# Kernel optimization log

Measured on AMD Instinct MI355X. Metric: run time of the kernel, lower is better.

Reference implementation:

```python
import jax, jax.numpy as jnp
import numpy as np

KH, KW = 3, 3  # window_size[1], window_size[2]
SH, SW = 1, 1  # strides
FILTERS = 64


def _extract_patches(x, kh, kw, sh, sw):
    # TF tf.image.extract_patches ordering: depth = (row, col, channel), channel fastest.
    B, H, W, C = x.shape
    Ho = (H - kh) // sh + 1
    Wo = (W - kw) // sw + 1
    # stack kh*kw shifted views -> (B, Ho, Wo, kh*kw, C)
    views = [x[:, i:i + (Ho - 1) * sh + 1:sh, j:j + (Wo - 1) * sw + 1:sw, :]
             for i in range(kh) for j in range(kw)]
    patches = jnp.stack(views, axis=3)
    return patches.reshape(B, Ho, Wo, kh * kw * C)


def setup_inputs() -> dict:
    key = jax.random.key(0)
    k1, k2 = jax.random.split(key)
    B, H, W, C = 8, 32, 32, 32
    K = KH * KW * C  # 288
    x = jax.random.normal(k1, (B, H, W, C), dtype=jnp.float32)
    w = jax.random.normal(k2, (1, 1, 1, K, FILTERS), dtype=jnp.float32) * 0.05
    bias = jnp.zeros((FILTERS,), dtype=jnp.float32)
    return {"x": x, "w": w, "bias": bias}


def reference(x, w, bias):
    # patches: (B, Ho, Wo, K)
    patches = _extract_patches(x, KH, KW, SH, SW)
    # broadcast add: (B, Ho, Wo, K, F)
    s = patches[..., None] + w
    # tropical max-plus minus min-plus over the patch axis, plus bias
    return jnp.max(s, axis=3) - jnp.min(s, axis=3) + bias
```

## Files before the change

### kernel.cpp

```cpp
#include <hip/hip_runtime.h>
#include <math.h>


#define PIX 2
#define TPB 256

__global__ __launch_bounds__(TPB) void trop_kernel(
    const float* __restrict__ x,
    const float* __restrict__ w,
    const float* __restrict__ bias,
    float* __restrict__ out)
{
    __shared__ float wlds[2][32 * 64];

    const int tid  = threadIdx.x;
    const int lane = tid & 63;
    const int wv   = tid >> 6;

    const int pix0 = blockIdx.x * (4 * PIX) + wv * PIX;

    const float* xp[PIX];
#pragma unroll
    for (int p = 0; p < PIX; ++p) {
        const int pid = pix0 + p;
        const int wo = pid % 30;
        const int t  = pid / 30;
        const int ho = t % 30;
        const int b  = t / 30;
        xp[p] = x + (((b * 32 + ho) * 32) + wo) * 32;
    }

    float amax[PIX], amin[PIX];
#pragma unroll
    for (int p = 0; p < PIX; ++p) { amax[p] = -INFINITY; amin[p] = INFINITY; }

    {
        const float4* src = (const float4*)w;
        ((float4*)wlds[0])[tid]       = src[tid];
        ((float4*)wlds[0])[tid + 256] = src[tid + 256];
    }
    __syncthreads();

#pragma unroll
    for (int tap = 0; tap < 9; ++tap) {
        const int cur = tap & 1;
        const int nxt = cur ^ 1;

        const int ntap = (tap < 8) ? tap + 1 : 8;
        const float4* src = (const float4*)(w + ntap * 2048);
        const float4 r0 = src[tid];
        const float4 r1 = src[tid + 256];

        const int dy = tap / 3;
        const int dx = tap % 3;
        const int xoff = (dy * 32 + dx) * 32;

#pragma unroll
        for (int c = 0; c < 32; c += 4) {
            const float w0 = wlds[cur][(c + 0) * 64 + lane];
            const float w1 = wlds[cur][(c + 1) * 64 + lane];
            const float w2 = wlds[cur][(c + 2) * 64 + lane];
            const float w3 = wlds[cur][(c + 3) * 64 + lane];
#pragma unroll
            for (int p = 0; p < PIX; ++p) {
                const float4 xv = *(const float4*)(xp[p] + xoff + c);
                const float s0 = xv.x + w0;
                const float s1 = xv.y + w1;
                const float s2 = xv.z + w2;
                const float s3 = xv.w + w3;
                amax[p] = fmaxf(fmaxf(fmaxf(fmaxf(amax[p], s0), s1), s2), s3);
                amin[p] = fminf(fminf(fminf(fminf(amin[p], s0), s1), s2), s3);
            }
        }

        ((float4*)wlds[nxt])[tid]       = r0;
        ((float4*)wlds[nxt])[tid + 256] = r1;
        __syncthreads();
    }

    const float bv = bias[lane];
#pragma unroll
    for (int p = 0; p < PIX; ++p)
        out[(pix0 + p) * 64 + lane] = amax[p] - amin[p] + bv;
}

extern "C" void kernel_launch(void* const* d_in, const int* in_sizes, int n_in,
                              void* d_out, int out_size, void* d_ws, size_t ws_size,
                              hipStream_t stream) {
    const float* x    = (const float*)d_in[0];
    const float* w    = (const float*)d_in[1];
    const float* bias = (const float*)d_in[2];
    float* out = (float*)d_out;

    trop_kernel<<<dim3(900), dim3(TPB), 0, stream>>>(x, w, bias, out);
}
```

Before: 77.79 us.

## Split channel reduction across waves with register-resident weights and LDS combine

Instead of each wave handling two pixels across all 288 patch elements with LDS double-buffered weights, each of 8 waves now owns a 4-channel slice of every tap and keeps its 36 weights in registers. Every wave processes 8 pixels, and the partial max/min values are combined through shared memory after a single barrier. This removes the per-tap LDS weight traffic and the nine barriers. In exchange it adds a cross-wave reduction and doubles the block size to 512 threads.

```diff
diff --git a/kernel.cpp b/kernel.cpp
--- a/kernel.cpp
+++ b/kernel.cpp
@@ -2,86 +2,83 @@
 #include <math.h>
 
 
-#define PIX 2
-#define TPB 256
+#define PPB 8
+#define NW  8
 
-__global__ __launch_bounds__(TPB) void trop_kernel(
+__global__ __launch_bounds__(512) void trop_kernel(
     const float* __restrict__ x,
     const float* __restrict__ w,
     const float* __restrict__ bias,
     float* __restrict__ out)
 {
-    __shared__ float wlds[2][32 * 64];
+    __shared__ float part[NW * PPB * 2 * 64];
 
     const int tid  = threadIdx.x;
     const int lane = tid & 63;
     const int wv   = tid >> 6;
+    const int pix0 = blockIdx.x * PPB;
 
-    const int pix0 = blockIdx.x * (4 * PIX) + wv * PIX;
+    float wr[36];
+#pragma unroll
+    for (int tap = 0; tap < 9; ++tap)
+#pragma unroll
+        for (int j = 0; j < 4; ++j)
+            wr[tap * 4 + j] = w[(tap * 32 + wv * 4 + j) * 64 + lane];
 
-    const float* xp[PIX];
+    const float* xb[PPB];
 #pragma unroll
-    for (int p = 0; p < PIX; ++p) {
+    for (int p = 0; p < PPB; ++p) {
         const int pid = pix0 + p;
         const int wo = pid % 30;
         const int t  = pid / 30;
         const int ho = t % 30;
         const int b  = t / 30;
-        xp[p] = x + (((b * 32 + ho) * 32) + wo) * 32;
+        xb[p] = x + (((b * 32 + ho) * 32) + wo) * 32 + wv * 4;
     }
 
-    float amax[PIX], amin[PIX];
+    float amax[PPB], amin[PPB];
 #pragma unroll
-    for (int p = 0; p < PIX; ++p) { amax[p] = -INFINITY; amin[p] = INFINITY; }
+    for (int p = 0; p < PPB; ++p) { amax[p] = -INFINITY; amin[p] = INFINITY; }
 
-    {
-        const float4* src = (const float4*)w;
-        ((float4*)wlds[0])[tid]       = src[tid];
-        ((float4*)wlds[0])[tid + 256] = src[tid + 256];
+#pragma unroll
+    for (int tap = 0; tap < 9; ++tap) {
+        const int dy = tap / 3;
+        const int dx = tap % 3;
+        const int xo = (dy * 32 + dx) * 32;
+
+        float4 xv[PPB];
+#pragma unroll
+        for (int p = 0; p < PPB; ++p)
+            xv[p] = *(const float4*)(xb[p] + xo);
+
+#pragma unroll
+        for (int p = 0; p < PPB; ++p) {
+            const float s0 = xv[p].x + wr[tap * 4 + 0];
+            const float s1 = xv[p].y + wr[tap * 4 + 1];
+            const float s2 = xv[p].z + wr[tap * 4 + 2];
+            const float s3 = xv[p].w + wr[tap * 4 + 3];
+            amax[p] = fmaxf(fmaxf(fmaxf(fmaxf(amax[p], s0), s1), s2), s3);
+            amin[p] = fminf(fminf(fminf(fminf(amin[p], s0), s1), s2), s3);
+        }
+    }
+
+#pragma unroll
+    for (int p = 0; p < PPB; ++p) {
+        part[((wv * PPB + p) * 2 + 0) * 64 + lane] = amax[p];
+        part[((wv * PPB + p) * 2 + 1) * 64 + lane] = amin[p];
     }
     __syncthreads();
 
+    {
+        const int p = wv;
+        float mx = -INFINITY, mn = INFINITY;
 #pragma unroll
-    for (int tap = 0; tap < 9; ++tap) {
-        const int cur = tap & 1;
-        const int nxt = cur ^ 1;
-
-        const int ntap = (tap < 8) ? tap + 1 : 8;
-        const float4* src = (const float4*)(w + ntap * 2048);
-        const float4 r0 = src[tid];
-        const float4 r1 = src[tid + 256];
-
-        const int dy = tap / 3;
-        const int dx = tap % 3;
-        const int xoff = (dy * 32 + dx) * 32;
-
-#pragma unroll
-        for (int c = 0; c < 32; c += 4) {
-            const float w0 = wlds[cur][(c + 0) * 64 + lane];
-            const float w1 = wlds[cur][(c + 1) * 64 + lane];
-            const float w2 = wlds[cur][(c + 2) * 64 + lane];
-            const float w3 = wlds[cur][(c + 3) * 64 + lane];
-#pragma unroll
-            for (int p = 0; p < PIX; ++p) {
-                const float4 xv = *(const float4*)(xp[p] + xoff + c);
-                const float s0 = xv.x + w0;
-                const float s1 = xv.y + w1;
-                const float s2 = xv.z + w2;
-                const float s3 = xv.w + w3;
-                amax[p] = fmaxf(fmaxf(fmaxf(fmaxf(amax[p], s0), s1), s2), s3);
-                amin[p] = fminf(fminf(fminf(fminf(amin[p], s0), s1), s2), s3);
-            }
+        for (int v = 0; v < NW; ++v) {
+            mx = fmaxf(mx, part[((v * PPB + p) * 2 + 0) * 64 + lane]);
+            mn = fminf(mn, part[((v * PPB + p) * 2 + 1) * 64 + lane]);
         }
-
-        ((float4*)wlds[nxt])[tid]       = r0;
-        ((float4*)wlds[nxt])[tid + 256] = r1;
-        __syncthreads();
+        out[(pix0 + p) * 64 + lane] = mx - mn + bias[lane];
     }
-
-    const float bv = bias[lane];
-#pragma unroll
-    for (int p = 0; p < PIX; ++p)
-        out[(pix0 + p) * 64 + lane] = amax[p] - amin[p] + bv;
 }
 
 extern "C" void kernel_launch(void* const* d_in, const int* in_sizes, int n_in,
@@ -92,5 +89,5 @@
     const float* bias = (const float*)d_in[2];
     float* out = (float*)d_out;
 
-    trop_kernel<<<dim3(900), dim3(TPB), 0, stream>>>(x, w, bias, out);
+    trop_kernel<<<dim3(900), dim3(512), 0, stream>>>(x, w, bias, out);
 }
```

Result: no change. 79.22 us (+1.8%).
